# Performance work log

Hardware: AMD Instinct MI355X
Metric: run time of the kernel (lower is better)

Reference implementation:

```python
import jax, jax.numpy as jnp
import numpy as np

N, K, H = 20000, 32, 128
DIN = 3 * H   # num_hidden + num_in = 128 + 256
FF = 4 * H
SCALE = 30.0
EPS = 1e-5


def setup_inputs() -> dict:
    key = jax.random.key(0)
    ks = jax.random.split(key, 32)
    s = 0.05
    w = lambda k, shp: jax.random.normal(k, shp, dtype=jnp.float32) * s
    return {
        "h_V": jax.random.normal(ks[0], (N, H), dtype=jnp.float32),
        "h_E": jax.random.normal(ks[1], (N, K, H), dtype=jnp.float32),
        "mask_V": jnp.ones((N,), dtype=jnp.float32),
        "mask_attend": jnp.ones((N, K), dtype=jnp.float32),
        # message MLP 1 (weights stored [in, out])
        "W1_w": w(ks[2], (DIN, H)), "W1_b": jnp.zeros((H,)),
        "W2_w": w(ks[3], (H, H)),   "W2_b": jnp.zeros((H,)),
        "W3_w": w(ks[4], (H, H)),   "W3_b": jnp.zeros((H,)),
        # message MLP 2
        "W11_w": w(ks[5], (DIN, H)), "W11_b": jnp.zeros((H,)),
        "W12_w": w(ks[6], (H, H)),   "W12_b": jnp.zeros((H,)),
        "W13_w": w(ks[7], (H, H)),   "W13_b": jnp.zeros((H,)),
        # position-wise FFN
        "Win_w": w(ks[8], (H, FF)),  "Win_b": jnp.zeros((FF,)),
        "Wout_w": w(ks[9], (FF, H)), "Wout_b": jnp.zeros((H,)),
        # LayerNorms
        "ln1_g": jnp.ones((H,)), "ln1_b": jnp.zeros((H,)),
        "ln2_g": jnp.ones((H,)), "ln2_b": jnp.zeros((H,)),
        "ln3_g": jnp.ones((H,)), "ln3_b": jnp.zeros((H,)),
        "E_idx": jax.random.randint(ks[10], (N, K), 0, N),
    }


def _ln(x, g, b):
    m = jnp.mean(x, -1, keepdims=True)
    v = jnp.mean(jnp.square(x - m), -1, keepdims=True)
    return (x - m) * jax.lax.rsqrt(v + EPS) * g + b


def _gelu(x):
    return jax.nn.gelu(x, approximate=False)  # torch default (erf) GELU


def reference(h_V, h_E, mask_V, mask_attend,
              W1_w, W1_b, W2_w, W2_b, W3_w, W3_b,
              W11_w, W11_b, W12_w, W12_b, W13_w, W13_b,
              Win_w, Win_b, Wout_w, Wout_b,
              ln1_g, ln1_b, ln2_g, ln2_b, ln3_g, ln3_b,
              E_idx):
    n, k = E_idx.shape

    def edge_feats(hv):
        nbr = hv[E_idx]  # [N,K,H] gather of neighbor node features
        hv_exp = jnp.broadcast_to(hv[:, None, :], (n, k, hv.shape[-1]))
        return jnp.concatenate([hv_exp, h_E, nbr], -1)  # [N,K,3H]

    # --- node update ---
    h_EV = edge_feats(h_V)
    msg = _gelu(h_EV @ W1_w + W1_b)
    msg = _gelu(msg @ W2_w + W2_b)
    msg = msg @ W3_w + W3_b
    msg = mask_attend[..., None] * msg
    dh = jnp.sum(msg, axis=-2) / SCALE
    hV = _ln(h_V + dh, ln1_g, ln1_b)
    dh = _gelu(hV @ Win_w + Win_b) @ Wout_w + Wout_b
    hV = _ln(hV + dh, ln2_g, ln2_b)
    hV = mask_V[:, None] * hV

    # --- edge update ---
    h_EV = edge_feats(hV)
    msg = _gelu(h_EV @ W11_w + W11_b)
    msg = _gelu(msg @ W12_w + W12_b)
    msg = msg @ W13_w + W13_b
    hE = _ln(h_E + msg, ln3_g, ln3_b)
    return (hV, hE)
```

## Files before the change

### kernel.cpp

```cpp
#include <hip/hip_runtime.h>
#include <hip/hip_bf16.h>
#include <cstdint>
#include <cstddef>

#define NN 20000
#define KK 32
#define HH 128
#define FFD 512
#define LN_EPS 1e-5f

typedef __attribute__((ext_vector_type(8))) short bf16x8;
typedef __attribute__((ext_vector_type(4))) float f32x4;

__device__ __forceinline__ short f2b(float f){
  __hip_bfloat16 h = __float2bfloat16(f);
  return __builtin_bit_cast(short, h);
}
__device__ __forceinline__ float b2f(short s){
  union { unsigned int u; float f; } v; v.u = ((unsigned int)(unsigned short)s) << 16; return v.f;
}
__device__ __forceinline__ unsigned int pk2(float a, float b){
  return (unsigned int)(unsigned short)f2b(a) | ((unsigned int)(unsigned short)f2b(b) << 16);
}
__device__ __forceinline__ float gelu_fast(float x){
  float u = x * __builtin_fmaf(0.10294278f, x*x, 2.3022082f);
  float e = __builtin_amdgcn_exp2f(u);
  float r = __builtin_amdgcn_rcpf(1.0f + e);
  return __builtin_fmaf(-x, r, x);
}
__device__ __forceinline__ f32x4 MFMA(bf16x8 a, bf16x8 b, f32x4 c){
  return __builtin_amdgcn_mfma_f32_16x16x32_bf16(a, b, c, 0, 0, 0);
}

__global__ __launch_bounds__(256) void enc_pack(
    const float* __restrict__ W1, const float* __restrict__ W2, const float* __restrict__ W3,
    const float* __restrict__ W11, const float* __restrict__ W12, const float* __restrict__ W13,
    const float* __restrict__ Win, const float* __restrict__ Wout,
    short* __restrict__ pk)
{
  const int stride = gridDim.x * blockDim.x;
  for (int idx = blockIdx.x*blockDim.x + threadIdx.x; idx < 294912; idx += stride){
    const float* src = W2; int srow = 0, k, n, NT, NCOLS, base;
    if (idx < 163840){
      int slot = idx >> 14, e = idx & 16383;
      k = e >> 7; n = e & 127; NT = 8; NCOLS = 128; base = slot << 14;
      switch (slot){
        case 0: src = W1;  srow = 0;   break;
        case 1: src = W1;  srow = 256; break;
        case 2: src = W1;  srow = 128; break;
        case 3: src = W2;  srow = 0;   break;
        case 4: src = W3;  srow = 0;   break;
        case 5: src = W11; srow = 0;   break;
        case 6: src = W11; srow = 256; break;
        case 7: src = W11; srow = 128; break;
        case 8: src = W12; srow = 0;   break;
        default: src = W13; srow = 0;  break;
      }
    } else if (idx < 229376){
      int e = idx - 163840; k = e >> 9; n = e & 511; NT = 32; NCOLS = 512; src = Win; base = 163840;
    } else {
      int e = idx - 229376; k = e >> 7; n = e & 127; NT = 8; NCOLS = 128; src = Wout; base = 229376;
    }
    float v = src[(srow + k)*NCOLS + n];
    int out = base + (((k>>5)*NT + (n>>4))*64 + ((k>>3)&3)*16 + (n&15))*8 + (k&7);
    pk[out] = f2b(v);
  }
}

__global__ __launch_bounds__(256, 2) void enc_proj(
    const float* __restrict__ X, const short* __restrict__ pkU, const short* __restrict__ pkZ,
    const float* __restrict__ biasU, short* __restrict__ U, short* __restrict__ Z)
{
  const int lane = threadIdx.x & 63, w = threadIdx.x >> 6;
  const int kgrp = lane >> 4, ccol = lane & 15;
  const int row0 = blockIdx.x*64 + w*16;
  const int arow = row0 + (lane & 15);
  f32x4 accU[8], accZ[8];
  #pragma unroll
  for (int nf=0;nf<8;nf++){ accU[nf] = (f32x4){0,0,0,0}; accZ[nf] = (f32x4){0,0,0,0}; }
  #pragma unroll
  for (int kt=0;kt<4;kt++){
    bf16x8 af = {0,0,0,0,0,0,0,0};
    if (arow < NN){
      const float4* p = (const float4*)(X + (size_t)arow*HH + kt*32 + kgrp*8);
      float4 v0 = p[0], v1 = p[1];
      af[0]=f2b(v0.x); af[1]=f2b(v0.y); af[2]=f2b(v0.z); af[3]=f2b(v0.w);
      af[4]=f2b(v1.x); af[5]=f2b(v1.y); af[6]=f2b(v1.z); af[7]=f2b(v1.w);
    }
    #pragma unroll
    for (int nf=0;nf<8;nf++){
      bf16x8 bu = *(const bf16x8*)(pkU + (((kt<<3)+nf)*64 + lane)*8);
      accU[nf] = MFMA(af, bu, accU[nf]);
      bf16x8 bz = *(const bf16x8*)(pkZ + (((kt<<3)+nf)*64 + lane)*8);
      accZ[nf] = MFMA(af, bz, accZ[nf]);
    }
  }
  #pragma unroll
  for (int nf=0;nf<8;nf++){
    #pragma unroll
    for (int r=0;r<4;r++){
      int grow = row0 + kgrp*4 + r;
      if (grow < NN){
        int col = nf*16 + ccol;
        U[(size_t)grow*HH + col] = f2b(accU[nf][r] + biasU[col]);
        Z[(size_t)grow*HH + col] = f2b(accZ[nf][r]);
      }
    }
  }
}

#define LSTR 136
template<int PASS>
__global__ __launch_bounds__(512, 4) void enc_mlp3(
    const float* __restrict__ hE,
    const short* __restrict__ Ub, const short* __restrict__ Zb,
    const int*  __restrict__ Eidx,
    const float* __restrict__ maskAtt,
    const float* __restrict__ hV,
    const float* __restrict__ lnG, const float* __restrict__ lnB,
    const short* __restrict__ pkL1,
    const short* __restrict__ pkL2, const float* __restrict__ bias2,
    const short* __restrict__ pkL3, const float* __restrict__ bias3,
    float* __restrict__ outP)
{
  __shared__ __align__(16) short sBuf[128*LSTR];
  __shared__ __align__(16) short sW[16384];
  __shared__ float sB23[256];
  __shared__ float sPart[8][128];

  const int i0 = blockIdx.x*4;
  const int t = threadIdx.x;
  const int lane = t & 63, w = t >> 6;
  const int kgrp = lane >> 4, ccol = lane & 15;
  const int node = i0 + (w >> 1);
  const int rw = w*16;

  if (t < 256) sB23[t] = (t < 128) ? bias2[t] : bias3[t-128];

  #pragma unroll
  for (int it=0; it<4; it++){
    int idx = it*512 + t;
    *(int4*)(sW + idx*8) = *(const int4*)(pkL1 + idx*8);
  }

  {
    const float4* src = (const float4*)(hE + ((size_t)i0*KK + rw)*HH);
    #pragma unroll
    for (int it=0; it<8; it++){
      int r = it*2 + (lane>>5);
      int c4 = lane & 31;
      float4 v = src[r*32 + c4];
      uint2 p; p.x = pk2(v.x, v.y); p.y = pk2(v.z, v.w);
      *(uint2*)(sBuf + (rw + r)*LSTR + c4*4) = p;
    }
  }
  __syncthreads();

  const short* sRow = sBuf + (rw + ccol)*LSTR;
  f32x4 acc[8];

  #pragma unroll
  for (int nf=0;nf<8;nf++) acc[nf] = (f32x4){0,0,0,0};
  #pragma unroll
  for (int kt=0;kt<4;kt++){
    bf16x8 af = *(const bf16x8*)(sRow + kt*32 + kgrp*8);
    #pragma unroll
    for (int nf=0;nf<8;nf++){
      bf16x8 b = *(const bf16x8*)(sW + (((kt<<3)+nf)*64 + lane)*8);
      acc[nf] = MFMA(af, b, acc[nf]);
    }
  }
  {
    const int zrow = rw + (lane >> 2);
    const int seg0 = lane & 3;
    const int jj = Eidx[i0*KK + zrow];
    const int4* zsrc = (const int4*)(Zb + (size_t)jj*HH);
    int4 z0 = zsrc[seg0];
    int4 z1 = zsrc[seg0 + 4];
    int4 z2 = zsrc[seg0 + 8];
    int4 z3 = zsrc[seg0 + 12];
    *(int4*)(sBuf + zrow*LSTR + (seg0     )*8) = z0;
    *(int4*)(sBuf + zrow*LSTR + (seg0 + 4 )*8) = z1;
    *(int4*)(sBuf + zrow*LSTR + (seg0 + 8 )*8) = z2;
    *(int4*)(sBuf + zrow*LSTR + (seg0 + 12)*8) = z3;
  }
  __syncthreads();
  #pragma unroll
  for (int it=0; it<4; it++){
    int idx = it*512 + t;
    *(int4*)(sW + idx*8) = *(const int4*)(pkL2 + idx*8);
  }
  #pragma unroll
  for (int nf=0;nf<8;nf++){
    float uv = b2f(Ub[(size_t)node*HH + nf*16 + ccol]);
    #pragma unroll
    for (int r=0;r<4;r++){
      short* p = sBuf + (rw + kgrp*4 + r)*LSTR + nf*16 + ccol;
      float v = acc[nf][r] + uv + b2f(*p);
      *p = f2b(gelu_fast(v));
    }
  }
  __syncthreads();

  #pragma unroll
  for (int nf=0;nf<8;nf++) acc[nf] = (f32x4){0,0,0,0};
  #pragma unroll
  for (int kt=0;kt<4;kt++){
    bf16x8 af = *(const bf16x8*)(sRow + kt*32 + kgrp*8);
    #pragma unroll
    for (int nf=0;nf<8;nf++){
      bf16x8 b = *(const bf16x8*)(sW + (((kt<<3)+nf)*64 + lane)*8);
      acc[nf] = MFMA(af, b, acc[nf]);
    }
  }
  __syncthreads();
  #pragma unroll
  for (int it=0; it<4; it++){
    int idx = it*512 + t;
    *(int4*)(sW + idx*8) = *(const int4*)(pkL3 + idx*8);
  }
  #pragma unroll
  for (int nf=0;nf<8;nf++){
    float b2v = sB23[nf*16 + ccol];
    #pragma unroll
    for (int r=0;r<4;r++){
      short* p = sBuf + (rw + kgrp*4 + r)*LSTR + nf*16 + ccol;
      *p = f2b(gelu_fast(acc[nf][r] + b2v));
    }
  }
  __syncthreads();

  #pragma unroll
  for (int nf=0;nf<8;nf++) acc[nf] = (f32x4){0,0,0,0};
  #pragma unroll
  for (int kt=0;kt<4;kt++){
    bf16x8 af = *(const bf16x8*)(sRow + kt*32 + kgrp*8);
    #pragma unroll
    for (int nf=0;nf<8;nf++){
      bf16x8 b = *(const bf16x8*)(sW + (((kt<<3)+nf)*64 + lane)*8);
      acc[nf] = MFMA(af, b, acc[nf]);
    }
  }

  if (PASS == 0){
    float m[4];
    {
      const float4 mv = *(const float4*)(maskAtt + i0*KK + rw + kgrp*4);
      m[0]=mv.x; m[1]=mv.y; m[2]=mv.z; m[3]=mv.w;
    }
    #pragma unroll
    for (int nf=0;nf<8;nf++){
      float b3v = sB23[128 + nf*16 + ccol];
      float s = 0.f;
      #pragma unroll
      for (int r=0;r<4;r++) s = __builtin_fmaf(acc[nf][r] + b3v, m[r], s);
      s += __shfl_xor(s, 16);
      s += __shfl_xor(s, 32);
      if (kgrp == 0) sPart[w][nf*16 + ccol] = s;
    }
    __syncthreads();
    if ((w & 1) == 0){
      float c0 = sPart[w][lane]    + sPart[w+1][lane];
      float c1 = sPart[w][64+lane] + sPart[w+1][64+lane];
      float x0 = hV[(size_t)node*HH + lane]      + c0*(1.0f/30.0f);
      float x1 = hV[(size_t)node*HH + 64 + lane] + c1*(1.0f/30.0f);
      float sm = x0 + x1, sq = x0*x0 + x1*x1;
      #pragma unroll
      for (int off=1; off<64; off<<=1){
        sm += __shfl_xor(sm, off);
        sq += __shfl_xor(sq, off);
      }
      float mean = sm*(1.f/128.f);
      float var  = sq*(1.f/128.f) - mean*mean;
      float inv  = rsqrtf(var + LN_EPS);
      outP[(size_t)node*HH + lane]      = (x0-mean)*inv*lnG[lane]    + lnB[lane];
      outP[(size_t)node*HH + 64 + lane] = (x1-mean)*inv*lnG[64+lane] + lnB[64+lane];
    }
  } else {
    float rs[4] = {0,0,0,0}, rq[4] = {0,0,0,0};
    #pragma unroll
    for (int nf=0;nf<8;nf++){
      float b3v = sB23[128 + nf*16 + ccol];
      #pragma unroll
      for (int r=0;r<4;r++){
        int row = rw + kgrp*4 + r, col = nf*16 + ccol;
        float x = acc[nf][r] + b3v + hE[((size_t)(i0*KK + row))*HH + col];
        acc[nf][r] = x;
        rs[r] += x; rq[r] += x*x;
      }
    }
    #pragma unroll
    for (int off=1; off<16; off<<=1){
      #pragma unroll
      for (int r=0;r<4;r++){
        rs[r] += __shfl_xor(rs[r], off);
        rq[r] += __shfl_xor(rq[r], off);
      }
    }
    #pragma unroll
    for (int r=0;r<4;r++){
      float mean = rs[r]*(1.f/128.f);
      float var  = rq[r]*(1.f/128.f) - mean*mean;
      float inv  = rsqrtf(var + LN_EPS);
      #pragma unroll
      for (int nf=0;nf<8;nf++){
        int row = rw + kgrp*4 + r, col = nf*16 + ccol;
        outP[((size_t)(i0*KK + row))*HH + col] = (acc[nf][r]-mean)*inv*lnG[col] + lnB[col];
      }
    }
  }
}

__global__ __launch_bounds__(256, 2) void enc_ffn(
    const float* __restrict__ X,
    const short* __restrict__ pkWin, const float* __restrict__ bin,
    const short* __restrict__ pkWout, const float* __restrict__ bout,
    const float* __restrict__ g2, const float* __restrict__ b2ln,
    const float* __restrict__ maskV,
    float* __restrict__ out)
{
  __shared__ short sT[64*512];
  const int t = threadIdx.x, lane = t & 63, w = t >> 6;
  const int kgrp = lane >> 4, ccol = lane & 15;
  const int row0 = blockIdx.x*64;
  const int arow = row0 + w*16 + (lane & 15);
  f32x4 acc[32];
  #pragma unroll
  for (int nf=0;nf<32;nf++) acc[nf] = (f32x4){0,0,0,0};
  #pragma unroll
  for (int kt=0;kt<4;kt++){
    bf16x8 af = {0,0,0,0,0,0,0,0};
    if (arow < NN){
      const float4* p = (const float4*)(X + (size_t)arow*HH + kt*32 + kgrp*8);
      float4 v0 = p[0], v1 = p[1];
      af[0]=f2b(v0.x); af[1]=f2b(v0.y); af[2]=f2b(v0.z); af[3]=f2b(v0.w);
      af[4]=f2b(v1.x); af[5]=f2b(v1.y); af[6]=f2b(v1.z); af[7]=f2b(v1.w);
    }
    #pragma unroll
    for (int nf=0;nf<32;nf++){
      bf16x8 b = *(const bf16x8*)(pkWin + ((size_t)((kt<<5)+nf)*64 + lane)*8);
      acc[nf] = MFMA(af, b, acc[nf]);
    }
  }
  #pragma unroll
  for (int nf=0;nf<32;nf++){
    #pragma unroll
    for (int r=0;r<4;r++){
      int rl = w*16 + kgrp*4 + r, col = nf*16 + ccol;
      sT[rl*512 + (col ^ ((rl&7)<<3))] = f2b(gelu_fast(acc[nf][r] + bin[col]));
    }
  }
  f32x4 a2[8];
  #pragma unroll
  for (int nf=0;nf<8;nf++) a2[nf] = (f32x4){0,0,0,0};
  const int rl_a = w*16 + (lane & 15);
  #pragma unroll
  for (int kt=0;kt<16;kt++){
    int base = kt*32 + kgrp*8;
    bf16x8 af = *(const bf16x8*)(sT + rl_a*512 + (base ^ ((rl_a&7)<<3)));
    #pragma unroll
    for (int nf=0;nf<8;nf++){
      bf16x8 b = *(const bf16x8*)(pkWout + (((kt<<3)+nf)*64 + lane)*8);
      a2[nf] = MFMA(af, b, a2[nf]);
    }
  }
  float rsum[4] = {0,0,0,0}, rsq[4] = {0,0,0,0};
  #pragma unroll
  for (int nf=0;nf<8;nf++){
    #pragma unroll
    for (int r=0;r<4;r++){
      int grow = row0 + w*16 + kgrp*4 + r, col = nf*16 + ccol;
      float prev = (grow < NN) ? X[(size_t)grow*HH + col] : 0.f;
      float x = a2[nf][r] + bout[col] + prev;
      a2[nf][r] = x;
      rsum[r] += x; rsq[r] += x*x;
    }
  }
  #pragma unroll
  for (int off=1; off<16; off<<=1){
    #pragma unroll
    for (int r=0;r<4;r++){
      rsum[r] += __shfl_xor(rsum[r], off);
      rsq[r]  += __shfl_xor(rsq[r], off);
    }
  }
  #pragma unroll
  for (int r=0;r<4;r++){
    int grow = row0 + w*16 + kgrp*4 + r;
    float mean = rsum[r]*(1.f/128.f);
    float var  = rsq[r]*(1.f/128.f) - mean*mean;
    float inv  = rsqrtf(var + LN_EPS);
    float mv   = (grow < NN) ? maskV[grow] : 0.f;
    #pragma unroll
    for (int nf=0;nf<8;nf++){
      int col = nf*16 + ccol;
      if (grow < NN)
        out[(size_t)grow*HH + col] = mv * ((a2[nf][r]-mean)*inv*g2[col] + b2ln[col]);
    }
  }
}

extern "C" void kernel_launch(void* const* d_in, const int* in_sizes, int n_in,
                              void* d_out, int out_size, void* d_ws, size_t ws_size,
                              hipStream_t stream)
{
  const float* h_V   = (const float*)d_in[0];
  const float* h_E   = (const float*)d_in[1];
  const float* maskV = (const float*)d_in[2];
  const float* maskA = (const float*)d_in[3];
  const float* W1w  = (const float*)d_in[4];  const float* W1b  = (const float*)d_in[5];
  const float* W2w  = (const float*)d_in[6];  const float* W2b  = (const float*)d_in[7];
  const float* W3w  = (const float*)d_in[8];  const float* W3b  = (const float*)d_in[9];
  const float* W11w = (const float*)d_in[10]; const float* W11b = (const float*)d_in[11];
  const float* W12w = (const float*)d_in[12]; const float* W12b = (const float*)d_in[13];
  const float* W13w = (const float*)d_in[14]; const float* W13b = (const float*)d_in[15];
  const float* Winw = (const float*)d_in[16]; const float* Winb = (const float*)d_in[17];
  const float* Woutw= (const float*)d_in[18]; const float* Woutb= (const float*)d_in[19];
  const float* ln1g = (const float*)d_in[20]; const float* ln1b = (const float*)d_in[21];
  const float* ln2g = (const float*)d_in[22]; const float* ln2b = (const float*)d_in[23];
  const float* ln3g = (const float*)d_in[24]; const float* ln3b = (const float*)d_in[25];
  const int*   Eidx = (const int*)d_in[26];

  float* outV = (float*)d_out;
  float* outE = outV + (size_t)NN*HH;

  char* ws = (char*)d_ws;
  short* pk = (short*)ws;
  const short* pkW1a  = pk + 0*16384;
  const short* pkW1c  = pk + 1*16384;
  const short* pkW1bb = pk + 2*16384;
  const short* pkW2   = pk + 3*16384;
  const short* pkW3   = pk + 4*16384;
  const short* pkW11a = pk + 5*16384;
  const short* pkW11c = pk + 6*16384;
  const short* pkW11bb= pk + 7*16384;
  const short* pkW12  = pk + 8*16384;
  const short* pkW13  = pk + 9*16384;
  const short* pkWin  = pk + 163840;
  const short* pkWout = pk + 229376;

  short* U1 = (short*)(ws + 1048576);
  short* Z1 = (short*)(ws + 6291456);
  short* U2 = (short*)(ws + 11534336);
  short* Z2 = (short*)(ws + 16777216);
  float* hVmid = (float*)(ws + 22020096);

  enc_pack<<<288, 256, 0, stream>>>(W1w, W2w, W3w, W11w, W12w, W13w, Winw, Woutw, pk);
  enc_proj<<<313, 256, 0, stream>>>(h_V, pkW1a, pkW1c, W1b, U1, Z1);
  enc_mlp3<0><<<NN/4, 512, 0, stream>>>(h_E, U1, Z1, Eidx, maskA, h_V,
                                        ln1g, ln1b, pkW1bb, pkW2, W2b, pkW3, W3b, hVmid);
  enc_ffn<<<313, 256, 0, stream>>>(hVmid, pkWin, Winb, pkWout, Woutb,
                                   ln2g, ln2b, maskV, outV);
  enc_proj<<<313, 256, 0, stream>>>(outV, pkW11a, pkW11c, W11b, U2, Z2);
  enc_mlp3<1><<<NN/4, 512, 0, stream>>>(h_E, U2, Z2, Eidx, nullptr, nullptr,
                                        ln3g, ln3b, pkW11bb, pkW12, W12b, pkW13, W13b, outE);
}
```

Baseline: 424.6 us.

## Make edge MLP kernel persistent with resident weights and prefetched next group

The edge-MLP kernel becomes persistent: a fixed grid of 256 blocks loops over groups of 4 nodes. All three layer weights are loaded into LDS once per block instead of being reloaded per layer per block. The next group's h_E tile and gathered Z rows are prefetched into registers while the current group computes. Block-wide barriers are removed except one around a double-buffered partial-sum array, since each wave only touches its own rows. The trade-off is much larger LDS use (about 130 KB per block) and more register pressure, which limits residency to one block of 8 waves per CU, so less latency can be hidden by occupancy.

```diff
diff --git a/kernel.cpp b/kernel.cpp
--- a/kernel.cpp
+++ b/kernel.cpp
@@ -8,6 +8,8 @@
 #define HH 128
 #define FFD 512
 #define LN_EPS 1e-5f
+#define NGRP 5000
+#define PGRID 256
 
 typedef __attribute__((ext_vector_type(8))) short bf16x8;
 typedef __attribute__((ext_vector_type(4))) float f32x4;
@@ -111,7 +113,7 @@
 
 #define LSTR 136
 template<int PASS>
-__global__ __launch_bounds__(512, 4) void enc_mlp3(
+__global__ __launch_bounds__(512, 2) void enc_mlp3(
     const float* __restrict__ hE,
     const short* __restrict__ Ub, const short* __restrict__ Zb,
     const int*  __restrict__ Eidx,
@@ -123,189 +125,203 @@
     const short* __restrict__ pkL3, const float* __restrict__ bias3,
     float* __restrict__ outP)
 {
+  __shared__ __align__(16) short sW1[16384];
+  __shared__ __align__(16) short sW2[16384];
+  __shared__ __align__(16) short sW3[16384];
   __shared__ __align__(16) short sBuf[128*LSTR];
-  __shared__ __align__(16) short sW[16384];
   __shared__ float sB23[256];
-  __shared__ float sPart[8][128];
-
-  const int i0 = blockIdx.x*4;
+  __shared__ float sPart[2][8][128];
+
   const int t = threadIdx.x;
   const int lane = t & 63, w = t >> 6;
   const int kgrp = lane >> 4, ccol = lane & 15;
-  const int node = i0 + (w >> 1);
   const int rw = w*16;
+  const int zrow = rw + (lane >> 2);
+  const int seg0 = lane & 3;
 
   if (t < 256) sB23[t] = (t < 128) ? bias2[t] : bias3[t-128];
-
   #pragma unroll
   for (int it=0; it<4; it++){
     int idx = it*512 + t;
-    *(int4*)(sW + idx*8) = *(const int4*)(pkL1 + idx*8);
-  }
-
-  {
-    const float4* src = (const float4*)(hE + ((size_t)i0*KK + rw)*HH);
+    *(int4*)(sW1 + idx*8) = *(const int4*)(pkL1 + idx*8);
+    *(int4*)(sW2 + idx*8) = *(const int4*)(pkL2 + idx*8);
+    *(int4*)(sW3 + idx*8) = *(const int4*)(pkL3 + idx*8);
+  }
+  __syncthreads();
+
+  const short* sRow = sBuf + (rw + ccol)*LSTR;
+  const int stg_r = (lane>>5);
+  const int stg_c = lane & 31;
+
+  int grp = blockIdx.x;
+  float4 pf[8];
+  int4 z0g, z1g, z2g, z3g;
+  if (grp < NGRP){
+    const float4* src = (const float4*)(hE + ((size_t)grp*128 + rw)*HH);
+    #pragma unroll
+    for (int it=0; it<8; it++) pf[it] = src[(it*2 + stg_r)*32 + stg_c];
+    int jj = Eidx[grp*128 + zrow];
+    const int4* zsrc = (const int4*)(Zb + (size_t)jj*HH);
+    z0g = zsrc[seg0]; z1g = zsrc[seg0+4]; z2g = zsrc[seg0+8]; z3g = zsrc[seg0+12];
+  }
+  int pb = 0;
+
+  for (; grp < NGRP; grp += PGRID){
+    const int nxt = grp + PGRID;
+    const size_t ebase = (size_t)grp*128;
+    const int node = grp*4 + (w >> 1);
+
     #pragma unroll
     for (int it=0; it<8; it++){
-      int r = it*2 + (lane>>5);
-      int c4 = lane & 31;
-      float4 v = src[r*32 + c4];
-      uint2 p; p.x = pk2(v.x, v.y); p.y = pk2(v.z, v.w);
-      *(uint2*)(sBuf + (rw + r)*LSTR + c4*4) = p;
-    }
-  }
-  __syncthreads();
-
-  const short* sRow = sBuf + (rw + ccol)*LSTR;
-  f32x4 acc[8];
-
-  #pragma unroll
-  for (int nf=0;nf<8;nf++) acc[nf] = (f32x4){0,0,0,0};
-  #pragma unroll
-  for (int kt=0;kt<4;kt++){
-    bf16x8 af = *(const bf16x8*)(sRow + kt*32 + kgrp*8);
+      uint2 p; p.x = pk2(pf[it].x, pf[it].y); p.y = pk2(pf[it].z, pf[it].w);
+      *(uint2*)(sBuf + (rw + it*2 + stg_r)*LSTR + stg_c*4) = p;
+    }
+    if (nxt < NGRP){
+      const float4* srcn = (const float4*)(hE + ((size_t)nxt*128 + rw)*HH);
+      #pragma unroll
+      for (int it=0; it<8; it++) pf[it] = srcn[(it*2 + stg_r)*32 + stg_c];
+    }
+    int jn = 0;
+    if (nxt < NGRP) jn = Eidx[nxt*128 + zrow];
+    float ureg[8];
+    #pragma unroll
+    for (int nf=0; nf<8; nf++) ureg[nf] = b2f(Ub[(size_t)node*HH + nf*16 + ccol]);
+    float m[4];
+    if (PASS == 0){
+      const float4 mv = *(const float4*)(maskAtt + ebase + rw + kgrp*4);
+      m[0]=mv.x; m[1]=mv.y; m[2]=mv.z; m[3]=mv.w;
+    }
+
+    f32x4 acc[8];
+    #pragma unroll
+    for (int nf=0;nf<8;nf++) acc[nf] = (f32x4){0,0,0,0};
+    #pragma unroll
+    for (int kt=0;kt<4;kt++){
+      bf16x8 af = *(const bf16x8*)(sRow + kt*32 + kgrp*8);
+      #pragma unroll
+      for (int nf=0;nf<8;nf++){
+        bf16x8 b = *(const bf16x8*)(sW1 + (((kt<<3)+nf)*64 + lane)*8);
+        acc[nf] = MFMA(af, b, acc[nf]);
+      }
+    }
+    *(int4*)(sBuf + zrow*LSTR + (seg0     )*8) = z0g;
+    *(int4*)(sBuf + zrow*LSTR + (seg0 + 4 )*8) = z1g;
+    *(int4*)(sBuf + zrow*LSTR + (seg0 + 8 )*8) = z2g;
+    *(int4*)(sBuf + zrow*LSTR + (seg0 + 12)*8) = z3g;
+    if (nxt < NGRP){
+      const int4* zsn = (const int4*)(Zb + (size_t)jn*HH);
+      z0g = zsn[seg0]; z1g = zsn[seg0+4]; z2g = zsn[seg0+8]; z3g = zsn[seg0+12];
+    }
     #pragma unroll
     for (int nf=0;nf<8;nf++){
-      bf16x8 b = *(const bf16x8*)(sW + (((kt<<3)+nf)*64 + lane)*8);
-      acc[nf] = MFMA(af, b, acc[nf]);
-    }
-  }
-  {
-    const int zrow = rw + (lane >> 2);
-    const int seg0 = lane & 3;
-    const int jj = Eidx[i0*KK + zrow];
-    const int4* zsrc = (const int4*)(Zb + (size_t)jj*HH);
-    int4 z0 = zsrc[seg0];
-    int4 z1 = zsrc[seg0 + 4];
-    int4 z2 = zsrc[seg0 + 8];
-    int4 z3 = zsrc[seg0 + 12];
-    *(int4*)(sBuf + zrow*LSTR + (seg0     )*8) = z0;
-    *(int4*)(sBuf + zrow*LSTR + (seg0 + 4 )*8) = z1;
-    *(int4*)(sBuf + zrow*LSTR + (seg0 + 8 )*8) = z2;
-    *(int4*)(sBuf + zrow*LSTR + (seg0 + 12)*8) = z3;
-  }
-  __syncthreads();
-  #pragma unroll
-  for (int it=0; it<4; it++){
-    int idx = it*512 + t;
-    *(int4*)(sW + idx*8) = *(const int4*)(pkL2 + idx*8);
-  }
-  #pragma unroll
-  for (int nf=0;nf<8;nf++){
-    float uv = b2f(Ub[(size_t)node*HH + nf*16 + ccol]);
-    #pragma unroll
-    for (int r=0;r<4;r++){
-      short* p = sBuf + (rw + kgrp*4 + r)*LSTR + nf*16 + ccol;
-      float v = acc[nf][r] + uv + b2f(*p);
-      *p = f2b(gelu_fast(v));
-    }
-  }
-  __syncthreads();
-
-  #pragma unroll
-  for (int nf=0;nf<8;nf++) acc[nf] = (f32x4){0,0,0,0};
-  #pragma unroll
-  for (int kt=0;kt<4;kt++){
-    bf16x8 af = *(const bf16x8*)(sRow + kt*32 + kgrp*8);
+      #pragma unroll
+      for (int r=0;r<4;r++){
+        short* p = sBuf + (rw + kgrp*4 + r)*LSTR + nf*16 + ccol;
+        float v = acc[nf][r] + ureg[nf] + b2f(*p);
+        *p = f2b(gelu_fast(v));
+      }
+    }
+    float res[32];
+    if (PASS == 1){
+      #pragma unroll
+      for (int nf=0;nf<8;nf++){
+        #pragma unroll
+        for (int r=0;r<4;r++)
+          res[nf*4+r] = hE[(ebase + rw + kgrp*4 + r)*HH + nf*16 + ccol];
+      }
+    }
+    #pragma unroll
+    for (int nf=0;nf<8;nf++) acc[nf] = (f32x4){0,0,0,0};
+    #pragma unroll
+    for (int kt=0;kt<4;kt++){
+      bf16x8 af = *(const bf16x8*)(sRow + kt*32 + kgrp*8);
+      #pragma unroll
+      for (int nf=0;nf<8;nf++){
+        bf16x8 b = *(const bf16x8*)(sW2 + (((kt<<3)+nf)*64 + lane)*8);
+        acc[nf] = MFMA(af, b, acc[nf]);
+      }
+    }
     #pragma unroll
     for (int nf=0;nf<8;nf++){
-      bf16x8 b = *(const bf16x8*)(sW + (((kt<<3)+nf)*64 + lane)*8);
-      acc[nf] = MFMA(af, b, acc[nf]);
-    }
-  }
-  __syncthreads();
-  #pragma unroll
-  for (int it=0; it<4; it++){
-    int idx = it*512 + t;
-    *(int4*)(sW + idx*8) = *(const int4*)(pkL3 + idx*8);
-  }
-  #pragma unroll
-  for (int nf=0;nf<8;nf++){
-    float b2v = sB23[nf*16 + ccol];
-    #pragma unroll
-    for (int r=0;r<4;r++){
-      short* p = sBuf + (rw + kgrp*4 + r)*LSTR + nf*16 + ccol;
-      *p = f2b(gelu_fast(acc[nf][r] + b2v));
-    }
-  }
-  __syncthreads();
-
-  #pragma unroll
-  for (int nf=0;nf<8;nf++) acc[nf] = (f32x4){0,0,0,0};
-  #pragma unroll
-  for (int kt=0;kt<4;kt++){
-    bf16x8 af = *(const bf16x8*)(sRow + kt*32 + kgrp*8);
-    #pragma unroll
-    for (int nf=0;nf<8;nf++){
-      bf16x8 b = *(const bf16x8*)(sW + (((kt<<3)+nf)*64 + lane)*8);
-      acc[nf] = MFMA(af, b, acc[nf]);
-    }
-  }
-
-  if (PASS == 0){
-    float m[4];
-    {
-      const float4 mv = *(const float4*)(maskAtt + i0*KK + rw + kgrp*4);
-      m[0]=mv.x; m[1]=mv.y; m[2]=mv.z; m[3]=mv.w;
-    }
-    #pragma unroll
-    for (int nf=0;nf<8;nf++){
-      float b3v = sB23[128 + nf*16 + ccol];
-      float s = 0.f;
-      #pragma unroll
-      for (int r=0;r<4;r++) s = __builtin_fmaf(acc[nf][r] + b3v, m[r], s);
-      s += __shfl_xor(s, 16);
-      s += __shfl_xor(s, 32);
-      if (kgrp == 0) sPart[w][nf*16 + ccol] = s;
-    }
-    __syncthreads();
-    if ((w & 1) == 0){
-      float c0 = sPart[w][lane]    + sPart[w+1][lane];
-      float c1 = sPart[w][64+lane] + sPart[w+1][64+lane];
-      float x0 = hV[(size_t)node*HH + lane]      + c0*(1.0f/30.0f);
-      float x1 = hV[(size_t)node*HH + 64 + lane] + c1*(1.0f/30.0f);
-      float sm = x0 + x1, sq = x0*x0 + x1*x1;
-      #pragma unroll
-      for (int off=1; off<64; off<<=1){
-        sm += __shfl_xor(sm, off);
-        sq += __shfl_xor(sq, off);
-      }
-      float mean = sm*(1.f/128.f);
-      float var  = sq*(1.f/128.f) - mean*mean;
-      float inv  = rsqrtf(var + LN_EPS);
-      outP[(size_t)node*HH + lane]      = (x0-mean)*inv*lnG[lane]    + lnB[lane];
-      outP[(size_t)node*HH + 64 + lane] = (x1-mean)*inv*lnG[64+lane] + lnB[64+lane];
-    }
-  } else {
-    float rs[4] = {0,0,0,0}, rq[4] = {0,0,0,0};
-    #pragma unroll
-    for (int nf=0;nf<8;nf++){
-      float b3v = sB23[128 + nf*16 + ccol];
+      float b2v = sB23[nf*16 + ccol];
       #pragma unroll
       for (int r=0;r<4;r++){
-        int row = rw + kgrp*4 + r, col = nf*16 + ccol;
-        float x = acc[nf][r] + b3v + hE[((size_t)(i0*KK + row))*HH + col];
-        acc[nf][r] = x;
-        rs[r] += x; rq[r] += x*x;
-      }
-    }
-    #pragma unroll
-    for (int off=1; off<16; off<<=1){
+        short* p = sBuf + (rw + kgrp*4 + r)*LSTR + nf*16 + ccol;
+        *p = f2b(gelu_fast(acc[nf][r] + b2v));
+      }
+    }
+    #pragma unroll
+    for (int nf=0;nf<8;nf++) acc[nf] = (f32x4){0,0,0,0};
+    #pragma unroll
+    for (int kt=0;kt<4;kt++){
+      bf16x8 af = *(const bf16x8*)(sRow + kt*32 + kgrp*8);
+      #pragma unroll
+      for (int nf=0;nf<8;nf++){
+        bf16x8 b = *(const bf16x8*)(sW3 + (((kt<<3)+nf)*64 + lane)*8);
+        acc[nf] = MFMA(af, b, acc[nf]);
+      }
+    }
+
+    if (PASS == 0){
+      #pragma unroll
+      for (int nf=0;nf<8;nf++){
+        float b3v = sB23[128 + nf*16 + ccol];
+        float s = 0.f;
+        #pragma unroll
+        for (int r=0;r<4;r++) s = __builtin_fmaf(acc[nf][r] + b3v, m[r], s);
+        s += __shfl_xor(s, 16);
+        s += __shfl_xor(s, 32);
+        if (kgrp == 0) sPart[pb][w][nf*16 + ccol] = s;
+      }
+      __syncthreads();
+      if ((w & 1) == 0){
+        float c0 = sPart[pb][w][lane]    + sPart[pb][w+1][lane];
+        float c1 = sPart[pb][w][64+lane] + sPart[pb][w+1][64+lane];
+        float x0 = hV[(size_t)node*HH + lane]      + c0*(1.0f/30.0f);
+        float x1 = hV[(size_t)node*HH + 64 + lane] + c1*(1.0f/30.0f);
+        float sm = x0 + x1, sq = x0*x0 + x1*x1;
+        #pragma unroll
+        for (int off=1; off<64; off<<=1){
+          sm += __shfl_xor(sm, off);
+          sq += __shfl_xor(sq, off);
+        }
+        float mean = sm*(1.f/128.f);
+        float var  = sq*(1.f/128.f) - mean*mean;
+        float inv  = rsqrtf(var + LN_EPS);
+        outP[(size_t)node*HH + lane]      = (x0-mean)*inv*lnG[lane]    + lnB[lane];
+        outP[(size_t)node*HH + 64 + lane] = (x1-mean)*inv*lnG[64+lane] + lnB[64+lane];
+      }
+      pb ^= 1;
+    } else {
+      float rs[4] = {0,0,0,0}, rq[4] = {0,0,0,0};
+      #pragma unroll
+      for (int nf=0;nf<8;nf++){
+        float b3v = sB23[128 + nf*16 + ccol];
+        #pragma unroll
+        for (int r=0;r<4;r++){
+          float x = acc[nf][r] + b3v + res[nf*4+r];
+          acc[nf][r] = x;
+          rs[r] += x; rq[r] += x*x;
+        }
+      }
+      #pragma unroll
+      for (int off=1; off<16; off<<=1){
+        #pragma unroll
+        for (int r=0;r<4;r++){
+          rs[r] += __shfl_xor(rs[r], off);
+          rq[r] += __shfl_xor(rq[r], off);
+        }
+      }
       #pragma unroll
       for (int r=0;r<4;r++){
-        rs[r] += __shfl_xor(rs[r], off);
-        rq[r] += __shfl_xor(rq[r], off);
-      }
-    }
-    #pragma unroll
-    for (int r=0;r<4;r++){
-      float mean = rs[r]*(1.f/128.f);
-      float var  = rq[r]*(1.f/128.f) - mean*mean;
-      float inv  = rsqrtf(var + LN_EPS);
-      #pragma unroll
-      for (int nf=0;nf<8;nf++){
-        int row = rw + kgrp*4 + r, col = nf*16 + ccol;
-        outP[((size_t)(i0*KK + row))*HH + col] = (acc[nf][r]-mean)*inv*lnG[col] + lnB[col];
+        float mean = rs[r]*(1.f/128.f);
+        float var  = rq[r]*(1.f/128.f) - mean*mean;
+        float inv  = rsqrtf(var + LN_EPS);
+        #pragma unroll
+        for (int nf=0;nf<8;nf++){
+          outP[(ebase + rw + kgrp*4 + r)*HH + nf*16 + ccol] =
+              (acc[nf][r]-mean)*inv*lnG[nf*16 + ccol] + lnB[nf*16 + ccol];
+        }
       }
     }
   }
@@ -447,11 +463,11 @@
 
   enc_pack<<<288, 256, 0, stream>>>(W1w, W2w, W3w, W11w, W12w, W13w, Winw, Woutw, pk);
   enc_proj<<<313, 256, 0, stream>>>(h_V, pkW1a, pkW1c, W1b, U1, Z1);
-  enc_mlp3<0><<<NN/4, 512, 0, stream>>>(h_E, U1, Z1, Eidx, maskA, h_V,
-                                        ln1g, ln1b, pkW1bb, pkW2, W2b, pkW3, W3b, hVmid);
+  enc_mlp3<0><<<PGRID, 512, 0, stream>>>(h_E, U1, Z1, Eidx, maskA, h_V,
+                                         ln1g, ln1b, pkW1bb, pkW2, W2b, pkW3, W3b, hVmid);
   enc_ffn<<<313, 256, 0, stream>>>(hVmid, pkWin, Winb, pkWout, Woutb,
                                    ln2g, ln2b, maskV, outV);
   enc_proj<<<313, 256, 0, stream>>>(outV, pkW11a, pkW11c, W11b, U2, Z2);
-  enc_mlp3<1><<<NN/4, 512, 0, stream>>>(h_E, U2, Z2, Eidx, nullptr, nullptr,
-                                        ln3g, ln3b, pkW11bb, pkW12, W12b, pkW13, W13b, outE);
-}
+  enc_mlp3<1><<<PGRID, 512, 0, stream>>>(h_E, U2, Z2, Eidx, nullptr, nullptr,
+                                         ln3g, ln3b, pkW11bb, pkW12, W12b, pkW13, W13b, outE);
+}
```

Measured after the change: 440.6 us. 3.8% more time.
